# Performance work log

Measured on AMD Instinct MI355X. Metric: run time of the kernel, lower is better.

## Reference

```python
import jax, jax.numpy as jnp
import numpy as np

N_NODES = 50000
N_EDGES = 800000
N_GRAPHS = 256
DIMS = [64, 128, 256, 512]
GRU_H = 256


def _linit(key, shape, fan_in):
    lim = 1.0 / np.sqrt(fan_in)
    return jax.random.uniform(key, shape, jnp.float32, -lim, lim)


def setup_inputs() -> dict:
    key = jax.random.key(0)
    ks = jax.random.split(key, 24)
    x = jax.random.normal(ks[0], (N_NODES, DIMS[0]), jnp.float32)
    edge_index = jax.random.randint(ks[1], (2, N_EDGES), 0, N_NODES, jnp.int64)
    batch_idx = jnp.sort(jax.random.randint(ks[2], (N_NODES,), 0, N_GRAPHS, jnp.int64))
    inp = {"x": x, "edge_index": edge_index, "batch_idx": batch_idx}
    # GCN layer weights (stored [in, out]) and biases
    for i in range(3):
        inp[f"gcn_w{i}"] = _linit(ks[3 + i], (DIMS[i], DIMS[i + 1]), DIMS[i])
        inp[f"gcn_b{i}"] = jnp.zeros((DIMS[i + 1],), jnp.float32)
    # gate nn: Linear(512, 1)
    inp["gate_w"] = _linit(ks[6], (DIMS[3], 1), DIMS[3])
    inp["gate_b"] = jnp.zeros((1,), jnp.float32)
    # GRU: 2 layers, torch layout W_ih [3H, in], W_hh [3H, H]
    ins = [DIMS[3], GRU_H]
    for l in range(2):
        inp[f"gru_wih{l}"] = _linit(ks[7 + 4 * l], (3 * GRU_H, ins[l]), GRU_H)
        inp[f"gru_whh{l}"] = _linit(ks[8 + 4 * l], (3 * GRU_H, GRU_H), GRU_H)
        inp[f"gru_bih{l}"] = _linit(ks[9 + 4 * l], (3 * GRU_H,), GRU_H)
        inp[f"gru_bhh{l}"] = _linit(ks[10 + 4 * l], (3 * GRU_H,), GRU_H)
    # output proj: Linear(256, 512), torch layout [out, in]
    inp["proj_w"] = _linit(ks[15], (DIMS[3], GRU_H), GRU_H)
    inp["proj_b"] = jnp.zeros((DIMS[3],), jnp.float32)
    return inp


def _gcn_norm(edge_index, n_nodes):
    # add self-loops, symmetric normalization (PyG GCNConv default)
    loop = jnp.arange(n_nodes, dtype=edge_index.dtype)
    src = jnp.concatenate([edge_index[0], loop])
    dst = jnp.concatenate([edge_index[1], loop])
    deg = jax.ops.segment_sum(jnp.ones_like(dst, jnp.float32), dst, num_segments=n_nodes)
    dinv = jnp.where(deg > 0, jax.lax.rsqrt(jnp.maximum(deg, 1.0)), 0.0)
    norm = dinv[src] * dinv[dst]
    return src, dst, norm


def _gru_cell(xv, h, wih, whh, bih, bhh):
    gi = xv @ wih.T + bih
    gh = h @ whh.T + bhh
    ir, iz, inn = jnp.split(gi, 3, axis=-1)
    hr, hz, hn = jnp.split(gh, 3, axis=-1)
    r = jax.nn.sigmoid(ir + hr)
    z = jax.nn.sigmoid(iz + hz)
    n = jnp.tanh(inn + r * hn)
    return (1.0 - z) * n + z * h


def reference(x, edge_index, batch_idx,
              gcn_w0, gcn_b0, gcn_w1, gcn_b1, gcn_w2, gcn_b2,
              gate_w, gate_b,
              gru_wih0, gru_whh0, gru_bih0, gru_bhh0,
              gru_wih1, gru_whh1, gru_bih1, gru_bhh1,
              proj_w, proj_b):
    n = x.shape[0]
    src, dst, norm = _gcn_norm(edge_index, n)
    for w, b in ((gcn_w0, gcn_b0), (gcn_w1, gcn_b1), (gcn_w2, gcn_b2)):
        h = x @ w                                  # [N, out]
        msg = h[src] * norm[:, None]               # gather over edges
        x = jax.ops.segment_sum(msg, dst, num_segments=n) + b
        x = jax.nn.relu(x)
    # attentional aggregation: segment softmax over gate scores
    gate = (x @ gate_w + gate_b)[:, 0]             # [N]
    gmax = jax.ops.segment_max(gate, batch_idx, num_segments=N_GRAPHS)
    e = jnp.exp(gate - gmax[batch_idx])
    denom = jax.ops.segment_sum(e, batch_idx, num_segments=N_GRAPHS)
    alpha = e / denom[batch_idx]
    graph_emb = jax.ops.segment_sum(x * alpha[:, None], batch_idx, num_segments=N_GRAPHS)  # [G, 512]
    # 2-layer GRU with seq_len=1, h0=0
    h0 = jnp.zeros((N_GRAPHS, GRU_H), x.dtype)
    h1 = _gru_cell(graph_emb, h0, gru_wih0, gru_whh0, gru_bih0, gru_bhh0)
    h2 = _gru_cell(h1, h0, gru_wih1, gru_whh1, gru_bih1, gru_bhh1)
    return h2 @ proj_w.T + proj_b                  # [G, 512]
```

## Files before the change

kernel.cpp:

```cpp
#include <hip/hip_runtime.h>


#define N_GRAPHS 256
#define GRU_H 256
#define SCAN_CHUNK 2048

typedef __attribute__((ext_vector_type(8))) short short8;
typedef __attribute__((ext_vector_type(4))) float floatx4;

typedef unsigned short ushort_t;
typedef unsigned int uint_t;

__device__ __forceinline__ float bflo(uint_t u) { return __uint_as_float(u << 16); }
__device__ __forceinline__ float bfhi(uint_t u) { return __uint_as_float(u & 0xffff0000u); }
__device__ __forceinline__ uint_t f2bf(float f) {
    uint_t u = __float_as_uint(f);
    return (u + 0x7fffu + ((u >> 16) & 1u)) >> 16;
}
__device__ __forceinline__ uint_t pack2(float a, float b) {
    return f2bf(a) | (f2bf(b) << 16);
}


__global__ void k_hist(const int* __restrict__ dst, int* __restrict__ counts, int E) {
    int e = blockIdx.x * blockDim.x + threadIdx.x;
    if (e < E) atomicAdd(&counts[dst[e]], 1);
}

__global__ __launch_bounds__(256) void k_scan1(const int* __restrict__ counts,
                                               int* __restrict__ rowptr,
                                               int* __restrict__ bsums,
                                               float* __restrict__ dinv, int n) {
    int b = blockIdx.x, t = threadIdx.x;
    int base = b * SCAN_CHUNK + t * 8;
    int v[8];
    int s = 0;
#pragma unroll
    for (int j = 0; j < 8; ++j) {
        int i = base + j;
        int c = (i < n) ? counts[i] : 0;
        v[j] = s;
        s += c;
        if (i < n) dinv[i] = rsqrtf((float)(c + 1));
    }
    __shared__ int sd[256];
    sd[t] = s;
    __syncthreads();
    for (int off = 1; off < 256; off <<= 1) {
        int tmp = (t >= off) ? sd[t - off] : 0;
        __syncthreads();
        sd[t] += tmp;
        __syncthreads();
    }
    int texcl = sd[t] - s;
    if (t == 255) bsums[b] = sd[255];
#pragma unroll
    for (int j = 0; j < 8; ++j) {
        int i = base + j;
        if (i < n) rowptr[i] = texcl + v[j];
    }
}

__global__ __launch_bounds__(256) void k_scan3(int* __restrict__ rowptr,
                                               int* __restrict__ cursor,
                                               const int* __restrict__ bsums,
                                               int n, int nb) {
    int b = blockIdx.x, t = threadIdx.x;
    __shared__ int s_off;
    if (t == 0) {
        int off = 0, tot = 0;
        for (int i = 0; i < nb; ++i) {
            int v = bsums[i];
            if (i < b) off += v;
            tot += v;
        }
        s_off = off;
        if (b == 0) rowptr[n] = tot;
    }
    __syncthreads();
    int off = s_off;
    int base = b * SCAN_CHUNK + t * 8;
#pragma unroll
    for (int j = 0; j < 8; ++j) {
        int i = base + j;
        if (i < n) { int r = rowptr[i] + off; rowptr[i] = r; cursor[i] = r; }
    }
}


__global__ __launch_bounds__(256) void k_pack(
    const int* __restrict__ src, const int* __restrict__ dst,
    int* __restrict__ cursor, int* __restrict__ col, int E,
    const float4* __restrict__ x, const float* __restrict__ dinv,
    uint4* __restrict__ xs, int N,
    const float* __restrict__ w0, const float* __restrict__ w1,
    const float* __restrict__ w2, ushort_t* __restrict__ wt0,
    ushort_t* __restrict__ wt1, ushort_t* __restrict__ wt2,
    const float* __restrict__ wih0, const float* __restrict__ wih1,
    const float* __restrict__ pw,
    ushort_t* __restrict__ sh0, ushort_t* __restrict__ sl0,
    ushort_t* __restrict__ sh1, ushort_t* __restrict__ sl1,
    ushort_t* __restrict__ sh2, ushort_t* __restrict__ sl2,
    int nf, int np, int nw) {
    int b = blockIdx.x, t = threadIdx.x;
    if (b < nf) {
        int e = b * 256 + t;
        if (e < E) {
            int pos = atomicAdd(&cursor[dst[e]], 1);
            col[pos] = src[e];
        }
    } else if (b < nf + np) {
        int idx = (b - nf) * 256 + t;
        int n = idx >> 3;
        if (n < N) {
            float dn = dinv[n];
            float4 v0 = x[idx * 2], v1 = x[idx * 2 + 1];
            uint4 o;
            o.x = pack2(v0.x * dn, v0.y * dn);
            o.y = pack2(v0.z * dn, v0.w * dn);
            o.z = pack2(v1.x * dn, v1.y * dn);
            o.w = pack2(v1.z * dn, v1.w * dn);
            xs[idx] = o;
        }
    } else if (b < nf + np + nw) {
        int idx = (b - nf - np) * 256 + t;
        if (idx < 8192) {
            int k = idx >> 7, n = idx & 127;
            wt0[(size_t)n * 64 + k] = (ushort_t)f2bf(w0[idx]);
        } else if (idx < 40960) {
            int i = idx - 8192;
            int k = i >> 8, n = i & 255;
            wt1[(size_t)n * 128 + k] = (ushort_t)f2bf(w1[i]);
        } else if (idx < 172032) {
            int i = idx - 40960;
            int k = i >> 9, n = i & 511;
            wt2[(size_t)n * 256 + k] = (ushort_t)f2bf(w2[i]);
        }
    } else {
        int idx = (b - nf - np - nw) * 256 + t;
        const float* s; ushort_t* H; ushort_t* L; int i;
        if (idx < 393216)      { s = wih0; H = sh0; L = sl0; i = idx; }
        else if (idx < 589824) { s = wih1; H = sh1; L = sl1; i = idx - 393216; }
        else if (idx < 720896) { s = pw;   H = sh2; L = sl2; i = idx - 589824; }
        else return;
        float v = s[i];
        uint_t h = f2bf(v);
        H[i] = (ushort_t)h;
        L[i] = (ushort_t)f2bf(v - __uint_as_float(h << 16));
    }
}


__device__ __forceinline__ void acc8(float& a0, float& a1, float& a2, float& a3,
                                     float& a4, float& a5, float& a6, float& a7,
                                     const uint4& v) {
    a0 += bflo(v.x); a1 += bfhi(v.x); a2 += bflo(v.y); a3 += bfhi(v.y);
    a4 += bflo(v.z); a5 += bfhi(v.z); a6 += bflo(v.w); a7 += bfhi(v.w);
}

__global__ void k_gather_bf16(const uint4* __restrict__ xs, const int* __restrict__ rp,
                              const int* __restrict__ col, const float* __restrict__ dinv,
                              uint4* __restrict__ agg, int N, int shift ) {
    int idx = blockIdx.x * blockDim.x + threadIdx.x;
    int n = idx >> shift;
    if (n >= N) return;
    int c = idx & ((1 << shift) - 1);
    int C8 = 1 << shift;
    int a = rp[n], b = rp[n + 1];
    uint4 u = xs[(size_t)n * C8 + c];
    float a0 = bflo(u.x), a1 = bfhi(u.x), a2 = bflo(u.y), a3 = bfhi(u.y);
    float a4 = bflo(u.z), a5 = bfhi(u.z), a6 = bflo(u.w), a7 = bfhi(u.w);
    int k = a;
    for (; k + 8 <= b; k += 8) {
        int ci[8];
#pragma unroll
        for (int j = 0; j < 8; ++j) ci[j] = col[k + j];
        uint4 v[8];
#pragma unroll
        for (int j = 0; j < 8; ++j) v[j] = xs[(size_t)ci[j] * C8 + c];
#pragma unroll
        for (int j = 0; j < 8; ++j)
            acc8(a0, a1, a2, a3, a4, a5, a6, a7, v[j]);
    }
    for (; k + 4 <= b; k += 4) {
        int ci[4];
#pragma unroll
        for (int j = 0; j < 4; ++j) ci[j] = col[k + j];
        uint4 v[4];
#pragma unroll
        for (int j = 0; j < 4; ++j) v[j] = xs[(size_t)ci[j] * C8 + c];
#pragma unroll
        for (int j = 0; j < 4; ++j)
            acc8(a0, a1, a2, a3, a4, a5, a6, a7, v[j]);
    }
    for (; k < b; ++k) {
        uint4 v = xs[(size_t)col[k] * C8 + c];
        acc8(a0, a1, a2, a3, a4, a5, a6, a7, v);
    }
    float dn = dinv[n];
    uint4 o;
    o.x = pack2(a0 * dn, a1 * dn);
    o.y = pack2(a2 * dn, a3 * dn);
    o.z = pack2(a4 * dn, a5 * dn);
    o.w = pack2(a6 * dn, a7 * dn);
    agg[idx] = o;
}


__global__ __launch_bounds__(256) void k_gather_chunked(
    const uint4* __restrict__ xs, const int* __restrict__ rp,
    const int* __restrict__ col, const float* __restrict__ dinv,
    uint4* __restrict__ agg, int N, int c8shift ,
    int cpgshift ) {
    int id = blockIdx.x;
    int g = id & 7;
    int nb = id >> 3;
    int t = threadIdx.x;
    int n = nb * (256 >> cpgshift) + (t >> cpgshift);
    if (n >= N) return;
    int c = (g << cpgshift) + (t & ((1 << cpgshift) - 1));
    size_t rowoff = ((size_t)n << c8shift) + c;
    int a = rp[n], b = rp[n + 1];
    uint4 u = xs[rowoff];
    float a0 = bflo(u.x), a1 = bfhi(u.x), a2 = bflo(u.y), a3 = bfhi(u.y);
    float a4 = bflo(u.z), a5 = bfhi(u.z), a6 = bflo(u.w), a7 = bfhi(u.w);
    int k = a;
    for (; k + 8 <= b; k += 8) {
        int ci[8];
#pragma unroll
        for (int j = 0; j < 8; ++j) ci[j] = col[k + j];
        uint4 v[8];
#pragma unroll
        for (int j = 0; j < 8; ++j) v[j] = xs[((size_t)ci[j] << c8shift) + c];
#pragma unroll
        for (int j = 0; j < 8; ++j)
            acc8(a0, a1, a2, a3, a4, a5, a6, a7, v[j]);
    }
    for (; k + 4 <= b; k += 4) {
        int ci[4];
#pragma unroll
        for (int j = 0; j < 4; ++j) ci[j] = col[k + j];
        uint4 v[4];
#pragma unroll
        for (int j = 0; j < 4; ++j) v[j] = xs[((size_t)ci[j] << c8shift) + c];
#pragma unroll
        for (int j = 0; j < 4; ++j)
            acc8(a0, a1, a2, a3, a4, a5, a6, a7, v[j]);
    }
    for (; k < b; ++k) {
        uint4 v = xs[((size_t)col[k] << c8shift) + c];
        acc8(a0, a1, a2, a3, a4, a5, a6, a7, v);
    }
    float dn = dinv[n];
    uint4 o;
    o.x = pack2(a0 * dn, a1 * dn);
    o.y = pack2(a2 * dn, a3 * dn);
    o.z = pack2(a4 * dn, a5 * dn);
    o.w = pack2(a6 * dn, a7 * dn);
    agg[rowoff] = o;
}


__global__ __launch_bounds__(256) void k_gemm_mfma(
    const ushort_t* __restrict__ A, const ushort_t* __restrict__ Wt,
    const float* __restrict__ bias, const float* __restrict__ dinv,
    ushort_t* __restrict__ C, int M, int K, int Nout, int scale_out,
    const float* __restrict__ gate_w, float* __restrict__ gateArr,
    int mB, int bnShift) {
    int id = blockIdx.x;
    int xcd = id & 7;
    int k2 = id >> 3;
    int bnI = k2 & ((1 << bnShift) - 1);
    int bmI = (k2 >> bnShift) * 8 + xcd;
    if (bmI >= mB) return;
    int bm = bmI * 64, bn = bnI * 64;

    __shared__ ushort_t As[64 * 72];
    __shared__ ushort_t Bs[64 * 72];
    int tid = threadIdx.x;
    int wave = tid >> 6, lane = tid & 63;
    int quad = lane >> 4, lr = lane & 15;
    int wm = (wave & 1) * 32, wn = (wave >> 1) * 32;

    floatx4 zero = {0.f, 0.f, 0.f, 0.f};
    floatx4 acc00 = zero, acc01 = zero, acc10 = zero, acc11 = zero;

    int r0 = tid >> 3,         ko0 = (tid & 7) * 8;
    int r1 = (tid + 256) >> 3, ko1 = ((tid + 256) & 7) * 8;

    for (int k0 = 0; k0 < K; k0 += 64) {
        int ar0 = min(bm + r0, M - 1);
        int ar1 = min(bm + r1, M - 1);
        uint4 av0 = *(const uint4*)(A + (size_t)ar0 * K + k0 + ko0);
        uint4 av1 = *(const uint4*)(A + (size_t)ar1 * K + k0 + ko1);
        uint4 bv0 = *(const uint4*)(Wt + (size_t)(bn + r0) * K + k0 + ko0);
        uint4 bv1 = *(const uint4*)(Wt + (size_t)(bn + r1) * K + k0 + ko1);
        __syncthreads();
        *(uint4*)&As[r0 * 72 + ko0] = av0;
        *(uint4*)&As[r1 * 72 + ko1] = av1;
        *(uint4*)&Bs[r0 * 72 + ko0] = bv0;
        *(uint4*)&Bs[r1 * 72 + ko1] = bv1;
        __syncthreads();
#pragma unroll
        for (int ks = 0; ks < 2; ++ks) {
            short8 af0 = *(short8*)&As[(wm + lr) * 72 + ks * 32 + quad * 8];
            short8 af1 = *(short8*)&As[(wm + 16 + lr) * 72 + ks * 32 + quad * 8];
            short8 bf0 = *(short8*)&Bs[(wn + lr) * 72 + ks * 32 + quad * 8];
            short8 bf1 = *(short8*)&Bs[(wn + 16 + lr) * 72 + ks * 32 + quad * 8];
            acc00 = __builtin_amdgcn_mfma_f32_16x16x32_bf16(af0, bf0, acc00, 0, 0, 0);
            acc01 = __builtin_amdgcn_mfma_f32_16x16x32_bf16(af0, bf1, acc01, 0, 0, 0);
            acc10 = __builtin_amdgcn_mfma_f32_16x16x32_bf16(af1, bf0, acc10, 0, 0, 0);
            acc11 = __builtin_amdgcn_mfma_f32_16x16x32_bf16(af1, bf1, acc11, 0, 0, 0);
        }
    }

    float gwv[2] = {0.f, 0.f};
    if (gate_w) {
        gwv[0] = gate_w[bn + wn + lr];
        gwv[1] = gate_w[bn + wn + 16 + lr];
    }
    float pg[2][4] = {};
#pragma unroll
    for (int mi = 0; mi < 2; ++mi) {
#pragma unroll
        for (int ni = 0; ni < 2; ++ni) {
            floatx4 acc = (mi == 0) ? (ni == 0 ? acc00 : acc01)
                                    : (ni == 0 ? acc10 : acc11);
            int col = bn + wn + ni * 16 + lr;
            float bcol = bias[col];
#pragma unroll
            for (int r = 0; r < 4; ++r) {
                int row = bm + wm + mi * 16 + quad * 4 + r;
                if (row < M) {
                    float v = acc[r] + bcol;
                    v = fmaxf(v, 0.0f);
                    if (gate_w) pg[mi][r] += v * gwv[ni];
                    if (scale_out) v *= dinv[row];
                    C[(size_t)row * Nout + col] = (ushort_t)f2bf(v);
                }
            }
        }
    }
    if (gate_w) {
#pragma unroll
        for (int mi = 0; mi < 2; ++mi) {
#pragma unroll
            for (int r = 0; r < 4; ++r) {
                float p = pg[mi][r];
                p += __shfl_down(p, 8, 16);
                p += __shfl_down(p, 4, 16);
                p += __shfl_down(p, 2, 16);
                p += __shfl_down(p, 1, 16);
                if (lr == 0) {
                    int row = bm + wm + mi * 16 + quad * 4 + r;
                    if (row < M) atomicAdd(&gateArr[row], p);
                }
            }
        }
    }
}


__global__ __launch_bounds__(256) void k_gemm3(
    const ushort_t* __restrict__ Ahi, const ushort_t* __restrict__ Alo,
    const ushort_t* __restrict__ Whi, const ushort_t* __restrict__ Wlo,
    const float* __restrict__ bias, float* __restrict__ C,
    int M, int K, int Nout) {
    __shared__ ushort_t AsH[64 * 72];
    __shared__ ushort_t AsL[64 * 72];
    __shared__ ushort_t BsH[64 * 72];
    __shared__ ushort_t BsL[64 * 72];
    int tid = threadIdx.x;
    int wave = tid >> 6, lane = tid & 63;
    int quad = lane >> 4, lr = lane & 15;
    int wm = (wave & 1) * 32, wn = (wave >> 1) * 32;
    int bm = blockIdx.x * 64, bn = blockIdx.y * 64;

    floatx4 zero = {0.f, 0.f, 0.f, 0.f};
    floatx4 acc00 = zero, acc01 = zero, acc10 = zero, acc11 = zero;

    int r0 = tid >> 3,         ko0 = (tid & 7) * 8;
    int r1 = (tid + 256) >> 3, ko1 = ((tid + 256) & 7) * 8;

    for (int k0 = 0; k0 < K; k0 += 64) {
        int ar0 = min(bm + r0, M - 1);
        int ar1 = min(bm + r1, M - 1);
        size_t a0o = (size_t)ar0 * K + k0 + ko0, a1o = (size_t)ar1 * K + k0 + ko1;
        size_t b0o = (size_t)(bn + r0) * K + k0 + ko0, b1o = (size_t)(bn + r1) * K + k0 + ko1;
        uint4 ah0 = *(const uint4*)(Ahi + a0o), ah1 = *(const uint4*)(Ahi + a1o);
        uint4 al0 = *(const uint4*)(Alo + a0o), al1 = *(const uint4*)(Alo + a1o);
        uint4 bh0 = *(const uint4*)(Whi + b0o), bh1 = *(const uint4*)(Whi + b1o);
        uint4 bl0 = *(const uint4*)(Wlo + b0o), bl1 = *(const uint4*)(Wlo + b1o);
        __syncthreads();
        *(uint4*)&AsH[r0 * 72 + ko0] = ah0; *(uint4*)&AsH[r1 * 72 + ko1] = ah1;
        *(uint4*)&AsL[r0 * 72 + ko0] = al0; *(uint4*)&AsL[r1 * 72 + ko1] = al1;
        *(uint4*)&BsH[r0 * 72 + ko0] = bh0; *(uint4*)&BsH[r1 * 72 + ko1] = bh1;
        *(uint4*)&BsL[r0 * 72 + ko0] = bl0; *(uint4*)&BsL[r1 * 72 + ko1] = bl1;
        __syncthreads();
#pragma unroll
        for (int ks = 0; ks < 2; ++ks) {
            int a0i = (wm + lr) * 72 + ks * 32 + quad * 8;
            int a1i = (wm + 16 + lr) * 72 + ks * 32 + quad * 8;
            int b0i = (wn + lr) * 72 + ks * 32 + quad * 8;
            int b1i = (wn + 16 + lr) * 72 + ks * 32 + quad * 8;
            short8 afh0 = *(short8*)&AsH[a0i], afh1 = *(short8*)&AsH[a1i];
            short8 afl0 = *(short8*)&AsL[a0i], afl1 = *(short8*)&AsL[a1i];
            short8 bfh0 = *(short8*)&BsH[b0i], bfh1 = *(short8*)&BsH[b1i];
            short8 bfl0 = *(short8*)&BsL[b0i], bfl1 = *(short8*)&BsL[b1i];
            acc00 = __builtin_amdgcn_mfma_f32_16x16x32_bf16(afh0, bfh0, acc00, 0, 0, 0);
            acc00 = __builtin_amdgcn_mfma_f32_16x16x32_bf16(afh0, bfl0, acc00, 0, 0, 0);
            acc00 = __builtin_amdgcn_mfma_f32_16x16x32_bf16(afl0, bfh0, acc00, 0, 0, 0);
            acc01 = __builtin_amdgcn_mfma_f32_16x16x32_bf16(afh0, bfh1, acc01, 0, 0, 0);
            acc01 = __builtin_amdgcn_mfma_f32_16x16x32_bf16(afh0, bfl1, acc01, 0, 0, 0);
            acc01 = __builtin_amdgcn_mfma_f32_16x16x32_bf16(afl0, bfh1, acc01, 0, 0, 0);
            acc10 = __builtin_amdgcn_mfma_f32_16x16x32_bf16(afh1, bfh0, acc10, 0, 0, 0);
            acc10 = __builtin_amdgcn_mfma_f32_16x16x32_bf16(afh1, bfl0, acc10, 0, 0, 0);
            acc10 = __builtin_amdgcn_mfma_f32_16x16x32_bf16(afl1, bfh0, acc10, 0, 0, 0);
            acc11 = __builtin_amdgcn_mfma_f32_16x16x32_bf16(afh1, bfh1, acc11, 0, 0, 0);
            acc11 = __builtin_amdgcn_mfma_f32_16x16x32_bf16(afh1, bfl1, acc11, 0, 0, 0);
            acc11 = __builtin_amdgcn_mfma_f32_16x16x32_bf16(afl1, bfh1, acc11, 0, 0, 0);
        }
    }

#pragma unroll
    for (int mi = 0; mi < 2; ++mi) {
#pragma unroll
        for (int ni = 0; ni < 2; ++ni) {
            floatx4 acc = (mi == 0) ? (ni == 0 ? acc00 : acc01)
                                    : (ni == 0 ? acc10 : acc11);
            int col = bn + wn + ni * 16 + lr;
            float bcol = bias ? bias[col] : 0.0f;
#pragma unroll
            for (int r = 0; r < 4; ++r) {
                int row = bm + wm + mi * 16 + quad * 4 + r;
                if (row < M)
                    C[(size_t)row * Nout + col] = acc[r] + bcol;
            }
        }
    }
}


__global__ void k_gru_ep(const float* __restrict__ gi, const float* __restrict__ bih,
                         const float* __restrict__ bhh,
                         ushort_t* __restrict__ hhi, ushort_t* __restrict__ hlo, int G) {
    int idx = blockIdx.x * blockDim.x + threadIdx.x;
    int g = idx >> 8, j = idx & 255;
    if (g >= G) return;
    const float* row = gi + (size_t)g * 768;
    float ir = row[j]       + bih[j]       + bhh[j];
    float iz = row[j + 256] + bih[j + 256] + bhh[j + 256];
    float in = row[j + 512] + bih[j + 512];
    float r = 1.0f / (1.0f + expf(-ir));
    float z = 1.0f / (1.0f + expf(-iz));
    float nn = tanhf(in + r * bhh[j + 512]);
    float h = (1.0f - z) * nn;
    uint_t hi = f2bf(h);
    hhi[idx] = (ushort_t)hi;
    hlo[idx] = (ushort_t)f2bf(h - __uint_as_float(hi << 16));
}


__global__ __launch_bounds__(256) void k_softmax_emb(
    const uint_t* __restrict__ x , const float* __restrict__ gate,
    const int* __restrict__ batch, int N,
    ushort_t* __restrict__ embH, ushort_t* __restrict__ embL) {
    int g = blockIdx.x;
    int s, e;
    {
        int lo = 0, hi = N;
        while (lo < hi) { int mid = (lo + hi) >> 1; if (batch[mid] < g) lo = mid + 1; else hi = mid; }
        s = lo;
        lo = s; hi = N;
        while (lo < hi) { int mid = (lo + hi) >> 1; if (batch[mid] < g + 1) lo = mid + 1; else hi = mid; }
        e = lo;
    }
    __shared__ float red[256];
    __shared__ float sal[256];
    int tid = threadIdx.x;
    float m = -INFINITY;
    for (int i = s + tid; i < e; i += 256) m = fmaxf(m, gate[i]);
    red[tid] = m; __syncthreads();
    for (int off = 128; off > 0; off >>= 1) {
        if (tid < off) red[tid] = fmaxf(red[tid], red[tid + off]);
        __syncthreads();
    }
    m = red[0]; __syncthreads();
    float ssum = 0.f;
    for (int i = s + tid; i < e; i += 256) ssum += expf(gate[i] - m);
    red[tid] = ssum; __syncthreads();
    for (int off = 128; off > 0; off >>= 1) {
        if (tid < off) red[tid] += red[tid + off];
        __syncthreads();
    }
    float denom = red[0];
    float inv = (denom > 0.f) ? 1.0f / denom : 0.0f;
    float acc0 = 0.f, acc1 = 0.f;
    for (int base = s; base < e; base += 256) {
        int i = base + tid;
        __syncthreads();
        sal[tid] = (i < e) ? expf(gate[i] - m) * inv : 0.0f;
        __syncthreads();
        int cnt = min(256, e - base);
        for (int k = 0; k < cnt; ++k) {
            float a = sal[k];
            uint_t u = x[(size_t)(base + k) * 256 + tid];
            acc0 += a * bflo(u);
            acc1 += a * bfhi(u);
        }
    }
    int i0 = g * 512 + tid * 2;
    uint_t h0 = f2bf(acc0);
    uint_t h1 = f2bf(acc1);
    embH[i0]     = (ushort_t)h0;
    embH[i0 + 1] = (ushort_t)h1;
    embL[i0]     = (ushort_t)f2bf(acc0 - __uint_as_float(h0 << 16));
    embL[i0 + 1] = (ushort_t)f2bf(acc1 - __uint_as_float(h1 << 16));
}


extern "C" void kernel_launch(void* const* d_in, const int* in_sizes, int n_in,
                              void* d_out, int out_size, void* d_ws, size_t ws_size,
                              hipStream_t stream) {
    const float* x       = (const float*)d_in[0];
    const int*   ei      = (const int*)d_in[1];
    const int*   batch   = (const int*)d_in[2];
    const float* w0      = (const float*)d_in[3];
    const float* b0      = (const float*)d_in[4];
    const float* w1      = (const float*)d_in[5];
    const float* b1      = (const float*)d_in[6];
    const float* w2      = (const float*)d_in[7];
    const float* b2      = (const float*)d_in[8];
    const float* gate_w  = (const float*)d_in[9];
    const float* wih0    = (const float*)d_in[11];
    const float* bih0    = (const float*)d_in[13];
    const float* bhh0    = (const float*)d_in[14];
    const float* wih1    = (const float*)d_in[15];
    const float* bih1    = (const float*)d_in[17];
    const float* bhh1    = (const float*)d_in[18];
    const float* pw      = (const float*)d_in[19];
    const float* pb      = (const float*)d_in[20];
    float* out = (float*)d_out;

    const int N = in_sizes[2];
    const int E = in_sizes[1] / 2;
    const int G = N_GRAPHS;

    char* base = (char*)d_ws;
    size_t off = 0;
    auto alloc = [&](size_t bytes) -> char* {
        char* p = base + off;
        off = (off + bytes + 255) & ~(size_t)255;
        return p;
    };
    ushort_t* bufA  = (ushort_t*)alloc((size_t)N * 512 * 2);
    ushort_t* bufB  = (ushort_t*)alloc((size_t)N * 512 * 2);
    float* dinv     = (float*)alloc((size_t)N * 4);
    float* gateArr  = (float*)alloc((size_t)N * 4);
    int*   counts   = (int*)alloc((size_t)(N + 1) * 4);
    int*   cursor   = (int*)alloc((size_t)(N + 1) * 4);
    int*   rowptr   = (int*)alloc((size_t)(N + 1) * 4);
    int*   bsums    = (int*)alloc((size_t)256 * 4);
    int*   col      = (int*)alloc((size_t)E * 4);
    ushort_t* wt0   = (ushort_t*)alloc((size_t)128 * 64 * 2);
    ushort_t* wt1   = (ushort_t*)alloc((size_t)256 * 128 * 2);
    ushort_t* wt2   = (ushort_t*)alloc((size_t)512 * 256 * 2);
    ushort_t* ih0H  = (ushort_t*)alloc((size_t)768 * 512 * 2);
    ushort_t* ih0L  = (ushort_t*)alloc((size_t)768 * 512 * 2);
    ushort_t* ih1H  = (ushort_t*)alloc((size_t)768 * 256 * 2);
    ushort_t* ih1L  = (ushort_t*)alloc((size_t)768 * 256 * 2);
    ushort_t* pwH   = (ushort_t*)alloc((size_t)512 * 256 * 2);
    ushort_t* pwL   = (ushort_t*)alloc((size_t)512 * 256 * 2);
    ushort_t* embH  = (ushort_t*)alloc((size_t)G * 512 * 2);
    ushort_t* embL  = (ushort_t*)alloc((size_t)G * 512 * 2);
    ushort_t* h1H   = (ushort_t*)alloc((size_t)G * 256 * 2);
    ushort_t* h1L   = (ushort_t*)alloc((size_t)G * 256 * 2);
    ushort_t* h2H   = (ushort_t*)alloc((size_t)G * 256 * 2);
    ushort_t* h2L   = (ushort_t*)alloc((size_t)G * 256 * 2);
    float* gi       = (float*)alloc((size_t)G * 768 * 4);
    (void)ws_size; (void)n_in; (void)out_size;

    const int* src = ei;
    const int* dst = ei + E;

    const int nb = (N + SCAN_CHUNK - 1) / SCAN_CHUNK;

    size_t zbytes = (size_t)((char*)counts - (char*)gateArr) + (size_t)(N + 1) * 4;
    hipMemsetAsync(gateArr, 0, zbytes, stream);

    k_hist<<<(E + 255) / 256, 256, 0, stream>>>(dst, counts, E);
    k_scan1<<<nb, 256, 0, stream>>>(counts, rowptr, bsums, dinv, N);
    k_scan3<<<nb, 256, 0, stream>>>(rowptr, cursor, bsums, N, nb);

    int nf = (E + 255) / 256;
    int np = (N * 8 + 255) / 256;
    int nw = (172032 + 255) / 256;
    int ns = (720896 + 255) / 256;
    k_pack<<<nf + np + nw + ns, 256, 0, stream>>>(
        src, dst, cursor, col, E,
        (const float4*)x, dinv, (uint4*)bufA, N,
        w0, w1, w2, wt0, wt1, wt2,
        wih0, wih1, pw, ih0H, ih0L, ih1H, ih1L, pwH, pwL,
        nf, np, nw);

    int mB = (N + 63) / 64;
    int mBpad = ((mB + 7) / 8) * 8;

    k_gather_bf16<<<(N * 8 + 255) / 256, 256, 0, stream>>>((const uint4*)bufA, rowptr, col, dinv, (uint4*)bufB, N, 3);
    k_gemm_mfma<<<mBpad * 2, 256, 0, stream>>>(bufB, wt0, b0, dinv, bufA, N, 64, 128, 1, nullptr, nullptr, mB, 1);

    int nb2 = (N + 127) / 128;
    k_gather_chunked<<<nb2 * 8, 256, 0, stream>>>((const uint4*)bufA, rowptr, col, dinv, (uint4*)bufB, N, 4, 1);
    k_gemm_mfma<<<mBpad * 4, 256, 0, stream>>>(bufB, wt1, b1, dinv, bufA, N, 128, 256, 1, nullptr, nullptr, mB, 2);

    int nb3 = (N + 63) / 64;
    k_gather_chunked<<<nb3 * 8, 256, 0, stream>>>((const uint4*)bufA, rowptr, col, dinv, (uint4*)bufB, N, 5, 2);
    k_gemm_mfma<<<mBpad * 8, 256, 0, stream>>>(bufB, wt2, b2, dinv, bufA, N, 256, 512, 0, gate_w, gateArr, mB, 3);

    k_softmax_emb<<<G, 256, 0, stream>>>((const uint_t*)bufA, gateArr, batch, N, embH, embL);

    k_gemm3<<<dim3(G / 64, 12), 256, 0, stream>>>(embH, embL, ih0H, ih0L, nullptr, gi, G, 512, 768);
    k_gru_ep<<<G, 256, 0, stream>>>(gi, bih0, bhh0, h1H, h1L, G);

    k_gemm3<<<dim3(G / 64, 12), 256, 0, stream>>>(h1H, h1L, ih1H, ih1L, nullptr, gi, G, 256, 768);
    k_gru_ep<<<G, 256, 0, stream>>>(gi, bih1, bhh1, h2H, h2L, G);

    k_gemm3<<<dim3(G / 64, 8), 256, 0, stream>>>(h2H, h2L, pwH, pwL, pb, out, G, 256, 512);
}
```

Baseline: 488.5 us.

## Split gather by source half and store GEMM outputs as 64-column planes

The CSR fill now places edges whose source lies in the lower node half at the front of each row and the rest at the back, so that after filling, cursor marks the split point. Layers 2 and 3 each run the gather twice, once per source half, with the second pass adding onto the first pass's bf16 output. The preceding GEMMs write their outputs as 64-column planes so each gather block reads a contiguous plane, aiming at better L2 locality for the random row reads. The cost is extra launches, a read-modify-write of the output, and an added bf16 rounding step between the two halves.

After: 450.2 us. 1.09x faster.

```diff
diff --git a/kernel.cpp b/kernel.cpp
--- a/kernel.cpp
+++ b/kernel.cpp
@@ -90,7 +90,9 @@
 
 __global__ __launch_bounds__(256) void k_pack(
     const int* __restrict__ src, const int* __restrict__ dst,
-    int* __restrict__ cursor, int* __restrict__ col, int E,
+    const int* __restrict__ rowptr, int* __restrict__ cursor,
+    int* __restrict__ bcnt, int S,
+    int* __restrict__ col, int E,
     const float4* __restrict__ x, const float* __restrict__ dinv,
     uint4* __restrict__ xs, int N,
     const float* __restrict__ w0, const float* __restrict__ w1,
@@ -106,8 +108,11 @@
     if (b < nf) {
         int e = b * 256 + t;
         if (e < E) {
-            int pos = atomicAdd(&cursor[dst[e]], 1);
-            col[pos] = src[e];
+            int d = dst[e], s = src[e];
+            int pos;
+            if (s < S) pos = atomicAdd(&cursor[d], 1);
+            else       pos = rowptr[d + 1] - 1 - atomicAdd(&bcnt[d], 1);
+            col[pos] = s;
         }
     } else if (b < nf + np) {
         int idx = (b - nf) * 256 + t;
@@ -207,23 +212,35 @@
 }
 
 
-__global__ __launch_bounds__(256) void k_gather_chunked(
-    const uint4* __restrict__ xs, const int* __restrict__ rp,
-    const int* __restrict__ col, const float* __restrict__ dinv,
-    uint4* __restrict__ agg, int N, int c8shift ,
-    int cpgshift ) {
+__global__ __launch_bounds__(256) void k_gather_split(
+    const uint4* __restrict__ xsP, const int* __restrict__ rp,
+    const int* __restrict__ split, const int* __restrict__ col,
+    const float* __restrict__ dinv, uint4* __restrict__ agg,
+    int N, int c8shift , int lgshift ,
+    int half, int dstChunk) {
     int id = blockIdx.x;
-    int g = id & 7;
+    int x = id & 7;
+    int q = x & ((1 << lgshift) - 1);
+    int dg = x >> lgshift;
     int nb = id >> 3;
     int t = threadIdx.x;
-    int n = nb * (256 >> cpgshift) + (t >> cpgshift);
-    if (n >= N) return;
-    int c = (g << cpgshift) + (t & ((1 << cpgshift) - 1));
-    size_t rowoff = ((size_t)n << c8shift) + c;
-    int a = rp[n], b = rp[n + 1];
-    uint4 u = xs[rowoff];
-    float a0 = bflo(u.x), a1 = bfhi(u.x), a2 = bflo(u.y), a3 = bfhi(u.y);
-    float a4 = bflo(u.z), a5 = bfhi(u.z), a6 = bflo(u.w), a7 = bfhi(u.w);
+    int n = dg * dstChunk + nb * 32 + (t >> 3);
+    if (n >= N || n >= (dg + 1) * dstChunk) return;
+    int lane8 = t & 7;
+    const uint4* plane = xsP + (size_t)q * (size_t)N * 8;
+    size_t outOff = ((size_t)n << c8shift) + (q << 3) + lane8;
+    int a = half ? split[n] : rp[n];
+    int b = half ? rp[n + 1] : split[n];
+    float a0, a1, a2, a3, a4, a5, a6, a7;
+    uint4 prev;
+    if (half) {
+        prev = agg[outOff];
+        a0 = a1 = a2 = a3 = a4 = a5 = a6 = a7 = 0.f;
+    } else {
+        uint4 u = plane[(size_t)n * 8 + lane8];
+        a0 = bflo(u.x); a1 = bfhi(u.x); a2 = bflo(u.y); a3 = bfhi(u.y);
+        a4 = bflo(u.z); a5 = bfhi(u.z); a6 = bflo(u.w); a7 = bfhi(u.w);
+    }
     int k = a;
     for (; k + 8 <= b; k += 8) {
         int ci[8];
@@ -231,7 +248,7 @@
         for (int j = 0; j < 8; ++j) ci[j] = col[k + j];
         uint4 v[8];
 #pragma unroll
-        for (int j = 0; j < 8; ++j) v[j] = xs[((size_t)ci[j] << c8shift) + c];
+        for (int j = 0; j < 8; ++j) v[j] = plane[(size_t)ci[j] * 8 + lane8];
 #pragma unroll
         for (int j = 0; j < 8; ++j)
             acc8(a0, a1, a2, a3, a4, a5, a6, a7, v[j]);
@@ -242,22 +259,29 @@
         for (int j = 0; j < 4; ++j) ci[j] = col[k + j];
         uint4 v[4];
 #pragma unroll
-        for (int j = 0; j < 4; ++j) v[j] = xs[((size_t)ci[j] << c8shift) + c];
+        for (int j = 0; j < 4; ++j) v[j] = plane[(size_t)ci[j] * 8 + lane8];
 #pragma unroll
         for (int j = 0; j < 4; ++j)
             acc8(a0, a1, a2, a3, a4, a5, a6, a7, v[j]);
     }
     for (; k < b; ++k) {
-        uint4 v = xs[((size_t)col[k] << c8shift) + c];
+        uint4 v = plane[(size_t)col[k] * 8 + lane8];
         acc8(a0, a1, a2, a3, a4, a5, a6, a7, v);
     }
     float dn = dinv[n];
     uint4 o;
-    o.x = pack2(a0 * dn, a1 * dn);
-    o.y = pack2(a2 * dn, a3 * dn);
-    o.z = pack2(a4 * dn, a5 * dn);
-    o.w = pack2(a6 * dn, a7 * dn);
-    agg[rowoff] = o;
+    if (half) {
+        o.x = pack2(bflo(prev.x) + a0 * dn, bfhi(prev.x) + a1 * dn);
+        o.y = pack2(bflo(prev.y) + a2 * dn, bfhi(prev.y) + a3 * dn);
+        o.z = pack2(bflo(prev.z) + a4 * dn, bfhi(prev.z) + a5 * dn);
+        o.w = pack2(bflo(prev.w) + a6 * dn, bfhi(prev.w) + a7 * dn);
+    } else {
+        o.x = pack2(a0 * dn, a1 * dn);
+        o.y = pack2(a2 * dn, a3 * dn);
+        o.z = pack2(a4 * dn, a5 * dn);
+        o.w = pack2(a6 * dn, a7 * dn);
+    }
+    agg[outOff] = o;
 }
 
 
@@ -266,7 +290,7 @@
     const float* __restrict__ bias, const float* __restrict__ dinv,
     ushort_t* __restrict__ C, int M, int K, int Nout, int scale_out,
     const float* __restrict__ gate_w, float* __restrict__ gateArr,
-    int mB, int bnShift) {
+    int mB, int bnShift, int planeC) {
     int id = blockIdx.x;
     int xcd = id & 7;
     int k2 = id >> 3;
@@ -319,6 +343,7 @@
         gwv[0] = gate_w[bn + wn + lr];
         gwv[1] = gate_w[bn + wn + 16 + lr];
     }
+    size_t m64 = (size_t)M * 64;
     float pg[2][4] = {};
 #pragma unroll
     for (int mi = 0; mi < 2; ++mi) {
@@ -336,7 +361,10 @@
                     v = fmaxf(v, 0.0f);
                     if (gate_w) pg[mi][r] += v * gwv[ni];
                     if (scale_out) v *= dinv[row];
-                    C[(size_t)row * Nout + col] = (ushort_t)f2bf(v);
+                    size_t cidx = planeC
+                        ? (size_t)(col >> 6) * m64 + (size_t)row * 64 + (col & 63)
+                        : (size_t)row * Nout + col;
+                    C[cidx] = (ushort_t)f2bf(v);
                 }
             }
         }
@@ -557,6 +585,7 @@
     ushort_t* bufB  = (ushort_t*)alloc((size_t)N * 512 * 2);
     float* dinv     = (float*)alloc((size_t)N * 4);
     float* gateArr  = (float*)alloc((size_t)N * 4);
+    int*   bcnt     = (int*)alloc((size_t)N * 4);
     int*   counts   = (int*)alloc((size_t)(N + 1) * 4);
     int*   cursor   = (int*)alloc((size_t)(N + 1) * 4);
     int*   rowptr   = (int*)alloc((size_t)(N + 1) * 4);
@@ -584,6 +613,7 @@
     const int* dst = ei + E;
 
     const int nb = (N + SCAN_CHUNK - 1) / SCAN_CHUNK;
+    const int S = N >> 1;
 
     size_t zbytes = (size_t)((char*)counts - (char*)gateArr) + (size_t)(N + 1) * 4;
     hipMemsetAsync(gateArr, 0, zbytes, stream);
@@ -597,7 +627,7 @@
     int nw = (172032 + 255) / 256;
     int ns = (720896 + 255) / 256;
     k_pack<<<nf + np + nw + ns, 256, 0, stream>>>(
-        src, dst, cursor, col, E,
+        src, dst, rowptr, cursor, bcnt, S, col, E,
         (const float4*)x, dinv, (uint4*)bufA, N,
         w0, w1, w2, wt0, wt1, wt2,
         wih0, wih1, pw, ih0H, ih0L, ih1H, ih1L, pwH, pwL,
@@ -607,15 +637,19 @@
     int mBpad = ((mB + 7) / 8) * 8;
 
     k_gather_bf16<<<(N * 8 + 255) / 256, 256, 0, stream>>>((const uint4*)bufA, rowptr, col, dinv, (uint4*)bufB, N, 3);
-    k_gemm_mfma<<<mBpad * 2, 256, 0, stream>>>(bufB, wt0, b0, dinv, bufA, N, 64, 128, 1, nullptr, nullptr, mB, 1);
-
-    int nb2 = (N + 127) / 128;
-    k_gather_chunked<<<nb2 * 8, 256, 0, stream>>>((const uint4*)bufA, rowptr, col, dinv, (uint4*)bufB, N, 4, 1);
-    k_gemm_mfma<<<mBpad * 4, 256, 0, stream>>>(bufB, wt1, b1, dinv, bufA, N, 128, 256, 1, nullptr, nullptr, mB, 2);
-
-    int nb3 = (N + 63) / 64;
-    k_gather_chunked<<<nb3 * 8, 256, 0, stream>>>((const uint4*)bufA, rowptr, col, dinv, (uint4*)bufB, N, 5, 2);
-    k_gemm_mfma<<<mBpad * 8, 256, 0, stream>>>(bufB, wt2, b2, dinv, bufA, N, 256, 512, 0, gate_w, gateArr, mB, 3);
+    k_gemm_mfma<<<mBpad * 2, 256, 0, stream>>>(bufB, wt0, b0, dinv, bufA, N, 64, 128, 1, nullptr, nullptr, mB, 1, 1);
+
+    int dc2 = (N + 3) / 4;
+    int g2 = ((dc2 + 31) / 32) * 8;
+    k_gather_split<<<g2, 256, 0, stream>>>((const uint4*)bufA, rowptr, cursor, col, dinv, (uint4*)bufB, N, 4, 1, 0, dc2);
+    k_gather_split<<<g2, 256, 0, stream>>>((const uint4*)bufA, rowptr, cursor, col, dinv, (uint4*)bufB, N, 4, 1, 1, dc2);
+    k_gemm_mfma<<<mBpad * 4, 256, 0, stream>>>(bufB, wt1, b1, dinv, bufA, N, 128, 256, 1, nullptr, nullptr, mB, 2, 1);
+
+    int dc3 = (N + 1) / 2;
+    int g3 = ((dc3 + 31) / 32) * 8;
+    k_gather_split<<<g3, 256, 0, stream>>>((const uint4*)bufA, rowptr, cursor, col, dinv, (uint4*)bufB, N, 5, 2, 0, dc3);
+    k_gather_split<<<g3, 256, 0, stream>>>((const uint4*)bufA, rowptr, cursor, col, dinv, (uint4*)bufB, N, 5, 2, 1, dc3);
+    k_gemm_mfma<<<mBpad * 8, 256, 0, stream>>>(bufB, wt2, b2, dinv, bufA, N, 256, 512, 0, gate_w, gateArr, mB, 3, 0);
 
     k_softmax_emb<<<G, 256, 0, stream>>>((const uint_t*)bufA, gateArr, batch, N, embH, embL);
 
```
